# Kernel tuning notes

Measured on AMD Instinct MI355X. Metric: run time of the kernel, lower is better.

The kernel has to match this reference:

```python
import jax, jax.numpy as jnp
import numpy as np

T = 10          # time_steps
IN_DIM = 784    # 28*28
HID = 256
NCLS = 47
THRESH = 1.0
TAU_MEM = 2.0   # LIF membrane time constant
TAU_OUT = 2.0   # readout EMA time constant


@jax.custom_vjp
def spike_fn(u):
    # Heaviside spike on (v - threshold), surrogate gradient in bwd.
    return (u >= 0.0).astype(u.dtype)

def _spike_fwd(u):
    return spike_fn(u), u

def _spike_bwd(u, g):
    # sigmoid surrogate derivative, slope 4
    s = jax.nn.sigmoid(4.0 * u)
    return (g * 4.0 * s * (1.0 - s),)

spike_fn.defvjp(_spike_fwd, _spike_bwd)


def setup_inputs() -> dict:
    key = jax.random.key(0)
    k1, k2, k3 = jax.random.split(key, 3)
    x = jax.random.uniform(k1, (4096, 1, 28, 28), dtype=jnp.float32)
    W1 = jax.random.normal(k2, (IN_DIM, HID), dtype=jnp.float32) / np.float32(np.sqrt(IN_DIM))
    b1 = jnp.zeros((HID,), jnp.float32)
    Wr = jax.random.normal(k3, (HID, NCLS), dtype=jnp.float32) / np.float32(np.sqrt(HID))
    br = jnp.zeros((NCLS,), jnp.float32)
    return {"x": x, "W1": W1, "b1": b1, "Wr": Wr, "br": br}


def reference(x, W1, b1, Wr, br):
    B = x.shape[0]
    xf = x.reshape(B, -1)  # [B, 784] pixel intensities in [0,1]
    # rate_encode_flat: Bernoulli(p=pixel) spikes per timestep -> [T, B, 784]
    ek = jax.random.key(42)
    seq = (jax.random.uniform(ek, (T, B, IN_DIM), dtype=xf.dtype) < xf[None]).astype(xf.dtype)

    def step(carry, s_t):
        v_hid, v_out = carry
        I_hid = s_t @ W1 + b1                      # [B, HID]
        v_hid = v_hid + (I_hid - v_hid) / TAU_MEM  # leaky integration
        spk = spike_fn(v_hid - THRESH)             # spike emission
        v_hid = v_hid * (1.0 - spk)                # hard reset to 0
        I = spk @ Wr + br                          # [B, NCLS]
        v_out = v_out + (I - v_out) / TAU_OUT      # output EMA
        return (v_hid, v_out), None

    init = (jnp.zeros((B, HID), xf.dtype), jnp.zeros((B, NCLS), xf.dtype))
    (_, v_out), _ = jax.lax.scan(step, init, seq)
    return v_out
```

## Files before the change

kernel.cpp:

```cpp
#include <hip/hip_runtime.h>
#include <stdint.h>


#define T_STEPS 10
#define BATCH   4096
#define IN_DIM  784
#define HID     256
#define NCLS    47
#define KWORDS  25
#define KPAD    800

#define WS_W1HI_OFF 46039040u
#define WS_W1MD_OFF (46039040u + 409600u)
#define WS_W1LO_OFF (46039040u + 819200u)

typedef __attribute__((ext_vector_type(8))) short    bf16x8;
typedef __attribute__((ext_vector_type(4))) float    f32x4;

__device__ __forceinline__ uint32_t rotl32(uint32_t x, uint32_t r) {
    return __builtin_amdgcn_alignbit(x, x, 32u - r);
}

__device__ __forceinline__ uint32_t tf_hash(uint32_t lo) {
    const uint32_t ks1 = 42u;
    const uint32_t ks2 = 0x1BD11BDAu ^ 42u;
    uint32_t x0 = 0u;
    uint32_t x1 = lo + ks1;
#define TF_RND(r) { x0 += x1; x1 = rotl32(x1, r); x1 ^= x0; }
    TF_RND(13) TF_RND(15) TF_RND(26) TF_RND(6)
    x0 += ks1; x1 += ks2 + 1u;
    TF_RND(17) TF_RND(29) TF_RND(16) TF_RND(24)
    x0 += ks2; x1 += 2u;
    TF_RND(13) TF_RND(15) TF_RND(26) TF_RND(6)
    x1 += ks1 + 3u;
    TF_RND(17) TF_RND(29) TF_RND(16) TF_RND(24)
    x0 += ks1; x1 += ks2 + 4u;
    TF_RND(13) TF_RND(15) TF_RND(26) TF_RND(6)
    x0 += ks2; x1 += 5u;
#undef TF_RND
    return x0 ^ x1;
}

__global__ __launch_bounds__(256) void splitk_k(
        const float* __restrict__ W1, ushort* __restrict__ hiT,
        ushort* __restrict__ midT, ushort* __restrict__ loT) {
    int n = blockIdx.x;
    for (int k = threadIdx.x; k < KPAD; k += 256) {
        float w = (k < IN_DIM) ? W1[k * HID + n] : 0.0f;
        uint32_t u = __float_as_uint(w);
        uint32_t hb = (u + 0x7FFFu + ((u >> 16) & 1u)) >> 16;
        float hf = __uint_as_float(hb << 16);
        float r1 = w - hf;
        uint32_t u1 = __float_as_uint(r1);
        uint32_t mb = (u1 + 0x7FFFu + ((u1 >> 16) & 1u)) >> 16;
        float mf2 = __uint_as_float(mb << 16);
        float r2 = r1 - mf2;
        uint32_t u2 = __float_as_uint(r2);
        uint32_t lb = (u2 + 0x7FFFu + ((u2 >> 16) & 1u)) >> 16;
        int kw = k >> 5, qk = (k >> 3) & 3, j = k & 7;
        size_t o = ((size_t)(kw * 256 + n) * 4 + qk) * 8 + j;
        hiT [o] = (ushort)hb;
        midT[o] = (ushort)mb;
        loT [o] = (ushort)lb;
    }
}

#define A_BUFSZ 5120
#define G_LDW   260

__global__ __launch_bounds__(512, 1) void fused_gemm_k(
        const ushort* __restrict__ hiT, const ushort* __restrict__ midT,
        const ushort* __restrict__ loT, const float* __restrict__ b1,
        const float* __restrict__ x, const float* __restrict__ Wr,
        const float* __restrict__ br, float* __restrict__ out) {
    __shared__ __align__(16) char lds[KWORDS * A_BUFSZ];

    const int tid = threadIdx.x;
    const int l   = tid & 63;
    const int wv  = tid >> 6;
    const int b0  = blockIdx.x << 3;

    f32x4 acc[5][2] = {};

    const int q   = l >> 4;
    const int c0  = l & 15;
    const int sig = q ^ (l & 3) ^ ((l >> 2) & 3);
    const int a_rd = (c0 << 6) + (sig << 4);

    const int beoff = ((wv << 5) + c0) * 32 + (q << 3);
    const ushort* bp_hi = hiT  + beoff;
    const ushort* bp_md = midT + beoff;
    const ushort* bp_lo = loT  + beoff;

    const int eL   = tid & 31;
    const int row0 = tid >> 5;
    const int j0   = row0 & 7;
    const int qd0  = ((eL >> 1) >> 2) ^ (row0 & 3) ^ ((row0 >> 2) & 3);
    const int adst0 = (row0 << 6) + (qd0 << 4) + (((eL >> 1) & 3) << 2)
                    + ((eL & 1) << 1);
    const int xbase = (b0 + j0) * IN_DIM + eL;
    const uint32_t tib0 = (uint32_t)((row0 >> 3) * BATCH + b0 + j0)
                        * (uint32_t)IN_DIM + (uint32_t)eL;

    {
        const float* xp = x + xbase;
        uint32_t ib = tib0;
#pragma unroll 1
        for (int kw = 0; kw < KWORDS; ++kw) {
            float xv = 0.0f;
            if (!(kw == KWORDS - 1 && eL >= 16))
                xv = xp[0];
            float xs = xv * 8388608.0f;
            char* ab = lds + kw * A_BUFSZ + adst0;
#pragma unroll
            for (int s = 0; s < 5; ++s) {
                uint32_t h = tf_hash(ib + (uint32_t)(s * 6422528));
                *(ushort*)(ab + (s << 10)) =
                    ((float)(h >> 9) < xs) ? (ushort)0x3F80 : (ushort)0;
            }
            xp += 32; ib += 32u;
        }
    }
    __syncthreads();

#pragma unroll 1
    for (int kw = 0; kw < KWORDS; ++kw) {
        bf16x8 bfr[3][2];
#pragma unroll
        for (int nt = 0; nt < 2; ++nt) {
            bfr[0][nt] = *(const bf16x8*)(bp_hi + nt * 512);
            bfr[1][nt] = *(const bf16x8*)(bp_md + nt * 512);
            bfr[2][nt] = *(const bf16x8*)(bp_lo + nt * 512);
        }
        bp_hi += 8192; bp_md += 8192; bp_lo += 8192;

        const char* A = lds + kw * A_BUFSZ;
        bf16x8 af[5];
#pragma unroll
        for (int mt = 0; mt < 5; ++mt)
            af[mt] = *(const bf16x8*)(A + a_rd + (mt << 10));

#pragma unroll
        for (int nt = 0; nt < 2; ++nt) {
#pragma unroll
            for (int mt = 0; mt < 5; ++mt) {
                acc[mt][nt] = __builtin_amdgcn_mfma_f32_16x16x32_bf16(af[mt], bfr[0][nt], acc[mt][nt], 0, 0, 0);
                acc[mt][nt] = __builtin_amdgcn_mfma_f32_16x16x32_bf16(af[mt], bfr[1][nt], acc[mt][nt], 0, 0, 0);
                acc[mt][nt] = __builtin_amdgcn_mfma_f32_16x16x32_bf16(af[mt], bfr[2][nt], acc[mt][nt], 0, 0, 0);
            }
        }
    }

    float b1v[2];
#pragma unroll
    for (int nt = 0; nt < 2; ++nt)
        b1v[nt] = b1[(wv << 5) + (nt << 4) + c0];

    float av[5][2][4];
#pragma unroll
    for (int mt = 0; mt < 5; ++mt)
#pragma unroll
        for (int nt = 0; nt < 2; ++nt)
#pragma unroll
            for (int rr = 0; rr < 4; ++rr)
                av[mt][nt][rr] = acc[mt][nt][rr] + b1v[nt];

    const int qh = q >> 1;
    float g[2][4];
#pragma unroll
    for (int nt = 0; nt < 2; ++nt) {
#pragma unroll
        for (int rr = 0; rr < 4; ++rr) {
            float v = 0.f, ga = 0.f, wt = 0.0009765625f;
#pragma unroll
            for (int m = 0; m < 5; ++m) {
                float pv = __shfl_xor(av[m][nt][rr], 32);
                float Ie = qh ? pv : av[m][nt][rr];
                float Io = qh ? av[m][nt][rr] : pv;
                v = v + (Ie - v) * 0.5f;
                if (v >= 1.0f) { ga += wt; v = 0.f; }
                wt += wt;
                v = v + (Io - v) * 0.5f;
                if (v >= 1.0f) { ga += wt; v = 0.f; }
                wt += wt;
            }
            g[nt][rr] = ga;
        }
    }

    __syncthreads();
    float* gbuf = (float*)lds;
    if (l < 32) {
#pragma unroll
        for (int nt = 0; nt < 2; ++nt)
#pragma unroll
            for (int rr = 0; rr < 4; ++rr) {
                int jj  = ((q & 1) << 2) + rr;
                int col = (wv << 5) + (nt << 4) + c0;
                gbuf[jj * G_LDW + col] = g[nt][rr];
            }
    }
    __syncthreads();

    {
        const int c = l;
        if (c < NCLS) {
            const float* gb = &gbuf[wv * G_LDW];
            float a = 0.f;
            for (int h4 = 0; h4 < 64; ++h4) {
                float w0 = Wr[((h4 << 2) + 0) * NCLS + c];
                float w1 = Wr[((h4 << 2) + 1) * NCLS + c];
                float w2 = Wr[((h4 << 2) + 2) * NCLS + c];
                float w3 = Wr[((h4 << 2) + 3) * NCLS + c];
                float4 gg = *(const float4*)&gb[h4 << 2];
                a = fmaf(gg.x, w0, a);
                a = fmaf(gg.y, w1, a);
                a = fmaf(gg.z, w2, a);
                a = fmaf(gg.w, w3, a);
            }
            out[(b0 + wv) * NCLS + c] = a + br[c] * 0.9990234375f;
        }
    }
}

extern "C" void kernel_launch(void* const* d_in, const int* in_sizes, int n_in,
                              void* d_out, int out_size, void* d_ws, size_t ws_size,
                              hipStream_t stream) {
    const float* x  = (const float*)d_in[0];
    const float* W1 = (const float*)d_in[1];
    const float* b1 = (const float*)d_in[2];
    const float* Wr = (const float*)d_in[3];
    const float* br = (const float*)d_in[4];
    float* out = (float*)d_out;

    ushort* w1hi  = (ushort*)((char*)d_ws + WS_W1HI_OFF);
    ushort* w1md  = (ushort*)((char*)d_ws + WS_W1MD_OFF);
    ushort* w1lo  = (ushort*)((char*)d_ws + WS_W1LO_OFF);

    splitk_k<<<HID, 256, 0, stream>>>(W1, w1hi, w1md, w1lo);
    fused_gemm_k<<<BATCH / 8, 512, 0, stream>>>(w1hi, w1md, w1lo, b1, x,
                                                Wr, br, out);
}
```

Baseline: 209.3 us.

## Pack spike matrix as ballot bitmasks in LDS to raise occupancy

```diff
diff --git a/kernel.cpp b/kernel.cpp
--- a/kernel.cpp
+++ b/kernel.cpp
@@ -16,6 +16,7 @@
 
 typedef __attribute__((ext_vector_type(8))) short    bf16x8;
 typedef __attribute__((ext_vector_type(4))) float    f32x4;
+typedef __attribute__((ext_vector_type(4))) uint32_t u32x4;
 
 __device__ __forceinline__ uint32_t rotl32(uint32_t x, uint32_t r) {
     return __builtin_amdgcn_alignbit(x, x, 32u - r);
@@ -65,15 +66,15 @@
     }
 }
 
-#define A_BUFSZ 5120
 #define G_LDW   260
 
-__global__ __launch_bounds__(512, 1) void fused_gemm_k(
+__global__ __launch_bounds__(512, 4) void fused_gemm_k(
         const ushort* __restrict__ hiT, const ushort* __restrict__ midT,
         const ushort* __restrict__ loT, const float* __restrict__ b1,
         const float* __restrict__ x, const float* __restrict__ Wr,
         const float* __restrict__ br, float* __restrict__ out) {
-    __shared__ __align__(16) char lds[KWORDS * A_BUFSZ];
+    __shared__ __align__(16) char lds[8448];
+    uint32_t* abits = (uint32_t*)lds;
 
     const int tid = threadIdx.x;
     const int l   = tid & 63;
@@ -84,45 +85,37 @@
 
     const int q   = l >> 4;
     const int c0  = l & 15;
-    const int sig = q ^ (l & 3) ^ ((l >> 2) & 3);
-    const int a_rd = (c0 << 6) + (sig << 4);
 
     const int beoff = ((wv << 5) + c0) * 32 + (q << 3);
     const ushort* bp_hi = hiT  + beoff;
     const ushort* bp_md = midT + beoff;
     const ushort* bp_lo = loT  + beoff;
 
-    const int eL   = tid & 31;
-    const int row0 = tid >> 5;
-    const int j0   = row0 & 7;
-    const int qd0  = ((eL >> 1) >> 2) ^ (row0 & 3) ^ ((row0 >> 2) & 3);
-    const int adst0 = (row0 << 6) + (qd0 << 4) + (((eL >> 1) & 3) << 2)
-                    + ((eL & 1) << 1);
-    const int xbase = (b0 + j0) * IN_DIM + eL;
-    const uint32_t tib0 = (uint32_t)((row0 >> 3) * BATCH + b0 + j0)
-                        * (uint32_t)IN_DIM + (uint32_t)eL;
-
     {
-        const float* xp = x + xbase;
-        uint32_t ib = tib0;
+        const int eL = l & 31;
+        int wl = wv * 250 + (l >> 5);
 #pragma unroll 1
-        for (int kw = 0; kw < KWORDS; ++kw) {
+        for (int it = 0; it < 125; ++it) {
+            int row = wl / 25;
+            int kw  = wl - row * 25;
+            int k   = (kw << 5) + eL;
+            int t   = row >> 3, j = row & 7;
             float xv = 0.0f;
-            if (!(kw == KWORDS - 1 && eL >= 16))
-                xv = xp[0];
-            float xs = xv * 8388608.0f;
-            char* ab = lds + kw * A_BUFSZ + adst0;
-#pragma unroll
-            for (int s = 0; s < 5; ++s) {
-                uint32_t h = tf_hash(ib + (uint32_t)(s * 6422528));
-                *(ushort*)(ab + (s << 10)) =
-                    ((float)(h >> 9) < xs) ? (ushort)0x3F80 : (ushort)0;
-            }
-            xp += 32; ib += 32u;
+            if (k < IN_DIM)
+                xv = x[(b0 + j) * IN_DIM + k];
+            uint32_t ii = (uint32_t)((t << 12) + b0 + j) * (uint32_t)IN_DIM
+                        + (uint32_t)k;
+            uint32_t h  = tf_hash(ii);
+            bool pred = (float)(h >> 9) < xv * 8388608.0f;
+            unsigned long long bal = __ballot(pred);
+            if ((l & 31) == 0)
+                abits[wl] = (uint32_t)((l < 32) ? bal : (bal >> 32));
+            wl += 2;
         }
     }
     __syncthreads();
 
+    const int qsh = q << 3;
 #pragma unroll 1
     for (int kw = 0; kw < KWORDS; ++kw) {
         bf16x8 bfr[3][2];
@@ -134,11 +127,18 @@
         }
         bp_hi += 8192; bp_md += 8192; bp_lo += 8192;
 
-        const char* A = lds + kw * A_BUFSZ;
         bf16x8 af[5];
 #pragma unroll
-        for (int mt = 0; mt < 5; ++mt)
-            af[mt] = *(const bf16x8*)(A + a_rd + (mt << 10));
+        for (int mt = 0; mt < 5; ++mt) {
+            uint32_t wrd = abits[(mt * 16 + c0) * 25 + kw];
+            uint32_t byt = (wrd >> qsh) & 0xFFu;
+            u32x4 v;
+            v.x = ((byt & 1u)   ? 0x3F80u : 0u) | ((byt & 2u)   ? 0x3F800000u : 0u);
+            v.y = ((byt & 4u)   ? 0x3F80u : 0u) | ((byt & 8u)   ? 0x3F800000u : 0u);
+            v.z = ((byt & 16u)  ? 0x3F80u : 0u) | ((byt & 32u)  ? 0x3F800000u : 0u);
+            v.w = ((byt & 64u)  ? 0x3F80u : 0u) | ((byt & 128u) ? 0x3F800000u : 0u);
+            af[mt] = *(bf16x8*)&v;
+        }
 
 #pragma unroll
         for (int nt = 0; nt < 2; ++nt) {
```

After: 225.4 us. 7.7% more time.
